# Kernel optimization log

Hardware: AMD Instinct MI355X
Metric: run time of the kernel (lower is better)

Reference implementation:

```python
import jax, jax.numpy as jnp
import numpy as np

B, P, K, L, F, KS, NCLS = 8, 4096, 20, 10, 32, 5, 40
N = B * P


def setup_inputs() -> dict:
    key = jax.random.key(0)
    k = jax.random.split(key, 5)
    return {
        "pos": jax.random.normal(k[0], (N, 3), jnp.float32),
        "Wsp": jax.random.normal(k[1], (KS ** 3, F), jnp.float32) * 0.1,
        "root": jax.random.normal(k[2], (F,), jnp.float32) * 0.1,
        "bias": jnp.zeros((F,), jnp.float32),
        "gamma": jnp.ones((F,), jnp.float32),
        "beta": jnp.zeros((F,), jnp.float32),
        "W1": jax.random.normal(k[3], (F, 256), jnp.float32) * 0.1,
        "b1": jnp.zeros((256,), jnp.float32),
        "W2": jax.random.normal(k[4], (256, NCLS), jnp.float32) * 0.1,
        "b2": jnp.zeros((NCLS,), jnp.float32),
    }


def _knn(pos):
    # per-graph brute-force knn (loop=False), neighbors sorted by distance
    pts = pos.reshape(B, P, 3)

    def one(p):
        d = jnp.sum((p[:, None, :] - p[None, :, :]) ** 2, -1)  # (P,P)
        d = d.at[jnp.arange(P), jnp.arange(P)].set(jnp.inf)
        return jax.lax.top_k(-d, K)[1]

    nbr = jax.vmap(one)(pts) + (jnp.arange(B) * P)[:, None, None]
    return nbr.reshape(N, K)


def _eig3(A):
    # power iteration with deflation (nr_iterations=5) on batched 3x3 symmetric mats
    def pi(M):
        v = jnp.full((M.shape[0], 3), np.float32(3.0 ** -0.5))
        for _ in range(5):
            v = jnp.einsum("nij,nj->ni", M, v)
            v = v / (jnp.linalg.norm(v, axis=-1, keepdims=True) + 1e-12)
        lam = jnp.einsum("ni,nij,nj->n", v, M, v)
        return lam, v

    l1, v1 = pi(A)
    _, v2 = pi(A - l1[:, None, None] * v1[:, :, None] * v1[:, None, :])
    v3 = jnp.cross(v1, v2)
    v3 = v3 / (jnp.linalg.norm(v3, axis=-1, keepdims=True) + 1e-12)
    return jnp.stack([v1, v2, v3], axis=1)  # rows = eigenvectors, V[:,2] = normal


def reference(pos, Wsp, root, bias, gamma, beta, W1, b1, W2, b2):
    nbr = _knn(pos)                               # (N,K)
    clusters = pos[nbr] - pos[:, None, :]         # (N,K,3) neighbor - center
    cov = jnp.einsum("nmc,nmd->ncd", clusters[:, :L], clusters[:, :L])
    V = _eig3(cov)                                # (N,3,3)
    dirc = jnp.einsum("nkc,ndc->nkd", clusters, V)  # clusters @ V^T
    signs = jnp.sign(dirc[:, :, 2].sum(1))
    dirc = dirc.at[:, :, 2].multiply(signs[:, None])
    max_abs = jnp.max(jnp.abs(dirc).reshape(N, -1), 1)
    dirc = dirc / max_abs[:, None, None] * 0.5 + 0.5  # pseudo coords in [0,1]

    # SplineConv, degree=1, open splines, dim=3, in_channels=1 (x=ones)
    v = dirc * (KS - 1)
    f = jnp.floor(v)
    frac = v - f
    fi = f.astype(jnp.int32)
    bits = jnp.array([[(s >> 2) & 1, (s >> 1) & 1, s & 1] for s in range(8)], jnp.int32)
    idx = jnp.clip(fi[:, :, None, :] + bits[None, None, :, :], 0, KS - 1)  # (N,K,8,3)
    wgt = jnp.where(bits[None, None] == 1, frac[:, :, None, :], 1.0 - frac[:, :, None, :])
    basis = wgt.prod(-1)                                          # (N,K,8)
    flat = (idx[..., 0] * KS + idx[..., 1]) * KS + idx[..., 2]    # (N,K,8)
    msg = jnp.einsum("nks,nksf->nf", basis, Wsp[flat]) / K        # mean aggregation
    node = msg + root + bias                                      # root weight on x=1

    # BatchNorm1d (training-mode batch stats, eps=1e-5)
    mu = node.mean(0)
    var = ((node - mu) ** 2).mean(0)
    xb = gamma * (node - mu) / jnp.sqrt(var + 1e-5) + beta

    out3 = xb[:, :, None] * V[:, 2][:, None, :]   # (N,F,3) scale normal direction
    y = jax.nn.sigmoid(out3)
    ys = y.reshape(-1, P, F).mean(1)              # (3B,F) as in torch .view
    y1 = jax.nn.elu(ys @ W1 + b1)
    return jax.nn.log_softmax(y1 @ W2 + b2, axis=1)
```

## Files before the change

### kernel.cpp

```cpp
#include <hip/hip_runtime.h>
#include <hip/hip_bf16.h>
#include <math.h>

#define BGR 8
#define PP 4096
#define NPTS 32768
#define KNN 20
#define LCOV 10
#define FF 32
#define KS 5
#define NCLS 40
#define NGROUP 24
#define GROUPLEN 131072

#define SPLIT 8
#define CHUNK (PP / SPLIT)
#define PTSBLK 128
#define KTHR 1024
#define NSLOT (KNN + 1)
#define MPAD NSLOT
#define SENT 0xFFFFFFFFu
#define SCELLS 4096
#define SCAP 12

__device__ inline unsigned umn(unsigned a, unsigned b) { return a < b ? a : b; }
__device__ inline unsigned umx(unsigned a, unsigned b) { return a > b ? a : b; }

__device__ inline void mat3vec(const float M[9], const float v[3], float w[3]) {
    w[0] = M[0] * v[0] + M[1] * v[1] + M[2] * v[2];
    w[1] = M[3] * v[0] + M[4] * v[1] + M[5] * v[2];
    w[2] = M[6] * v[0] + M[7] * v[1] + M[8] * v[2];
}

__device__ inline float pi3(const float M[9], float v[3]) {
    v[0] = v[1] = v[2] = 0.57735026918962576f;
#pragma unroll
    for (int it = 0; it < 5; ++it) {
        float w[3];
        mat3vec(M, v, w);
        float nrm = sqrtf(w[0] * w[0] + w[1] * w[1] + w[2] * w[2]) + 1e-12f;
        v[0] = w[0] / nrm;
        v[1] = w[1] / nrm;
        v[2] = w[2] / nrm;
    }
    float w[3];
    mat3vec(M, v, w);
    return v[0] * w[0] + v[1] * w[1] + v[2] * w[2];
}

__global__ __launch_bounds__(KTHR, 4) void knn_kernel(
    const float* __restrict__ pos, unsigned short* __restrict__ nbr16,
    float* __restrict__ Rbuf, float* __restrict__ v3out) {
    __shared__ float smem[4 * PP];
    __shared__ unsigned short mOrig[PP];
    __shared__ unsigned samp[PTSBLK * 24];
    __shared__ float Tseed[PTSBLK];
    __shared__ unsigned scr[KTHR / 64][SCAP][64];
    float* tx = smem;
    float* ty = smem + PP;
    float* tz = smem + 2 * PP;
    float* tw = smem + 3 * PP;
    unsigned short* lnbr = (unsigned short*)(smem + 3 * PP + 2816);

    int b = blockIdx.x >> 5;
    int blkInGraph = blockIdx.x & 31;
    const float* gp = pos + (size_t)b * PP * 3;
    int tid = threadIdx.x;
    int lane = tid & 63;
    int wid = tid >> 6;

    {
        unsigned* cnt = (unsigned*)smem;
        unsigned short* cellOf = (unsigned short*)(smem + 4096);
        unsigned* tsum = (unsigned*)(smem + 6144);
        for (int i = tid; i < SCELLS; i += KTHR) cnt[i] = 0u;
        __syncthreads();
        for (int i = tid; i < PP; i += KTHR) {
            float x = gp[i * 3 + 0];
            float y = gp[i * 3 + 1];
            float z = gp[i * 3 + 2];
            int cx = min(max((int)floorf((x + 4.0f) * 2.0f), 0), 15);
            int cy = min(max((int)floorf((y + 4.0f) * 2.0f), 0), 15);
            int cz = min(max((int)floorf((z + 4.0f) * 2.0f), 0), 15);
            unsigned m = 0;
#pragma unroll
            for (int bb = 0; bb < 4; ++bb)
                m |= (((unsigned)(cx >> bb) & 1u) << (3 * bb + 2)) |
                     (((unsigned)(cy >> bb) & 1u) << (3 * bb + 1)) |
                     (((unsigned)(cz >> bb) & 1u) << (3 * bb + 0));
            cellOf[i] = (unsigned short)m;
            atomicAdd(&cnt[m], 1u);
        }
        __syncthreads();
        unsigned c0 = cnt[4 * tid + 0];
        unsigned c1 = cnt[4 * tid + 1];
        unsigned c2 = cnt[4 * tid + 2];
        unsigned c3 = cnt[4 * tid + 3];
        unsigned local = c0 + c1 + c2 + c3;
        tsum[tid] = local;
        __syncthreads();
        for (int off = 1; off < 1024; off <<= 1) {
            unsigned v = (tid >= off) ? tsum[tid - off] : 0u;
            __syncthreads();
            tsum[tid] += v;
            __syncthreads();
        }
        unsigned base = tsum[tid] - local;
        cnt[4 * tid + 0] = base;
        cnt[4 * tid + 1] = base + c0;
        cnt[4 * tid + 2] = base + c0 + c1;
        cnt[4 * tid + 3] = base + c0 + c1 + c2;
        __syncthreads();
        for (int i = tid; i < PP; i += KTHR) {
            unsigned dst = atomicAdd(&cnt[cellOf[i]], 1u);
            mOrig[dst] = (unsigned short)i;
        }
    }
    __syncthreads();

    for (int i = tid; i < PP; i += KTHR) {
        float x = gp[i * 3 + 0];
        float y = gp[i * 3 + 1];
        float z = gp[i * 3 + 2];
        tx[i] = -2.0f * x;
        ty[i] = -2.0f * y;
        tz[i] = -2.0f * z;
        tw[i] = x * x + y * y + z * z;
    }
    __syncthreads();

    int eighth = tid >> 7;
    int pt = tid & (PTSBLK - 1);
    int qSlot = blkInGraph * PTSBLK + pt;
    int li = mOrig[qSlot];
    float px = -0.5f * tx[li];
    float py = -0.5f * ty[li];
    float pz = -0.5f * tz[li];
    float p2 = tw[li];
    int jbeg = eighth * CHUNK;

    {
        unsigned s0 = SENT, s1 = SENT, s2 = SENT;
#pragma unroll 4
        for (int c = 0; c < 32; ++c) {
            int base = jbeg + c * 16;
            float4 xv = *(const float4*)(tx + base);
            float4 yv = *(const float4*)(ty + base);
            float4 zv = *(const float4*)(tz + base);
            float4 wv = *(const float4*)(tw + base);
            float xa[4] = {xv.x, xv.y, xv.z, xv.w};
            float ya[4] = {yv.x, yv.y, yv.z, yv.w};
            float za[4] = {zv.x, zv.y, zv.z, zv.w};
            float wa[4] = {wv.x, wv.y, wv.z, wv.w};
#pragma unroll
            for (int u = 0; u < 4; ++u) {
                float dh = fmaf(px, xa[u], fmaf(py, ya[u], fmaf(pz, za[u], wa[u])));
                float d = fmaxf(dh + p2, 0.0f);
                unsigned key = (__float_as_uint(d) & 0xFFFFF000u)
                               | (unsigned)(base + u);
                if (base + u == li) key = SENT;
                unsigned t0 = umn(key, s0); key = umx(key, s0); s0 = t0;
                t0 = umn(key, s1); key = umx(key, s1); s1 = t0;
                s2 = umn(key, s2);
            }
        }
        unsigned* sdst = &samp[pt * 24 + eighth * 3];
        sdst[0] = s0; sdst[1] = s1; sdst[2] = s2;
    }
    __syncthreads();
    if (tid < PTSBLK) {
        unsigned g0 = 0, g1 = 0, g2 = 0, g3 = 0;
        const unsigned* ss = &samp[tid * 24];
#pragma unroll
        for (int i = 0; i < 24; ++i) {
            unsigned k = ss[i], a;
            a = umx(k, g0); k = umn(k, g0); g0 = a;
            a = umx(k, g1); k = umn(k, g1); g1 = a;
            a = umx(k, g2); k = umn(k, g2); g2 = a;
            g3 = umx(k, g3);
        }
        Tseed[tid] = __uint_as_float((g3 & 0xFFFFF000u) + 0x2000u);
    }
    __syncthreads();
    float seed_hat = Tseed[pt] - p2;

    unsigned bd[NSLOT];
#pragma unroll
    for (int k = 0; k < NSLOT; k++) bd[k] = SENT;
    float worst_hat = seed_hat;

    unsigned* scrW = &scr[wid][0][0];
    unsigned cnt = 0;

    auto drain = [&]() {
#pragma unroll
        for (int s = 0; s < SCAP; ++s) {
            if (!__any((int)cnt > s)) break;
            unsigned k = (s < (int)cnt) ? scrW[s * 64 + lane] : SENT;
#pragma unroll
            for (int i = 0; i < NSLOT; i++) {
                unsigned lo = umn(k, bd[i]);
                k = umx(k, bd[i]);
                bd[i] = lo;
            }
        }
        cnt = 0;
        unsigned wb = bd[NSLOT - 1];
        float nw = (wb == SENT) ? INFINITY
                                : __uint_as_float(wb & 0xFFFFF000u) - p2;
        worst_hat = fminf(nw, seed_hat);
    };

    for (int jj = jbeg; jj < jbeg + CHUNK; jj += 8) {
        float4 xv0 = *(const float4*)(tx + jj);
        float4 yv0 = *(const float4*)(ty + jj);
        float4 zv0 = *(const float4*)(tz + jj);
        float4 wv0 = *(const float4*)(tw + jj);
        float4 xv1 = *(const float4*)(tx + jj + 4);
        float4 yv1 = *(const float4*)(ty + jj + 4);
        float4 zv1 = *(const float4*)(tz + jj + 4);
        float4 wv1 = *(const float4*)(tw + jj + 4);
        float xa[8] = {xv0.x, xv0.y, xv0.z, xv0.w, xv1.x, xv1.y, xv1.z, xv1.w};
        float ya[8] = {yv0.x, yv0.y, yv0.z, yv0.w, yv1.x, yv1.y, yv1.z, yv1.w};
        float za[8] = {zv0.x, zv0.y, zv0.z, zv0.w, zv1.x, zv1.y, zv1.z, zv1.w};
        float wa[8] = {wv0.x, wv0.y, wv0.z, wv0.w, wv1.x, wv1.y, wv1.z, wv1.w};
#pragma unroll
        for (int u = 0; u < 8; u++) {
            float dh = fmaf(px, xa[u], fmaf(py, ya[u], fmaf(pz, za[u], wa[u])));
            if (dh < worst_hat) {
                float d = fmaxf(dh + p2, 0.0f);
                scrW[cnt * 64 + lane] = (__float_as_uint(d) & 0xFFFFF000u)
                                        | (unsigned)(jj + u);
                cnt++;
            }
        }
        if (__any(cnt >= 4u)) drain();
    }
    drain();

    __syncthreads();
    unsigned* mk = (unsigned*)smem;
    for (int h = 0; h < 2; h++) {
        if ((pt >> 6) == h) {
            int lpt = pt & 63;
#pragma unroll
            for (int k = 0; k < NSLOT; k++)
                mk[(eighth * 64 + lpt) * MPAD + k] = bd[k];
        }
        __syncthreads();
        if (tid < 64) {
            int p = tid;
            const unsigned* base = &mk[p * MPAD];
            int cur[SPLIT];
#pragma unroll
            for (int q = 0; q < SPLIT; q++) cur[q] = 0;
            int lpt2 = h * 64 + p;
            int gi = b * PP + (int)mOrig[blkInGraph * PTSBLK + lpt2];
#pragma unroll
            for (int t = 0; t < NSLOT; t++) {
                unsigned v[SPLIT];
#pragma unroll
                for (int q = 0; q < SPLIT; q++)
                    v[q] = base[q * 64 * MPAD + cur[q]];
                unsigned m = v[0];
#pragma unroll
                for (int q = 1; q < SPLIT; q++) m = umn(m, v[q]);
                if (t > 0) {
                    int local = (int)(m & 0xFFFu);
                    nbr16[(size_t)gi * KNN + (t - 1)] = (unsigned short)local;
                    lnbr[lpt2 * KNN + (t - 1)] = (unsigned short)local;
                }
#pragma unroll
                for (int q = 0; q < SPLIT; q++) cur[q] += (v[q] == m);
            }
        }
        __syncthreads();
    }

    for (int i = tid; i < PP; i += KTHR) {
        tx[i] = gp[i * 3 + 0];
        ty[i] = gp[i * 3 + 1];
        tz[i] = gp[i * 3 + 2];
    }
    __syncthreads();

    if (tid < PTSBLK) {
        int lp = tid;
        int ng = mOrig[blkInGraph * PTSBLK + lp];
        int n = b * PP + ng;
        float qx = tx[ng], qy = ty[ng], qz = tz[ng];
        const unsigned short* ln = &lnbr[lp * KNN];

        float m00 = 0.f, m01 = 0.f, m02 = 0.f, m11 = 0.f, m12 = 0.f, m22 = 0.f;
#pragma unroll
        for (int k = 0; k < LCOV; k++) {
            int id = ln[k];
            float cx = tx[id] - qx;
            float cy = ty[id] - qy;
            float cz = tz[id] - qz;
            m00 += cx * cx; m01 += cx * cy; m02 += cx * cz;
            m11 += cy * cy; m12 += cy * cz; m22 += cz * cz;
        }
        float M[9] = {m00, m01, m02, m01, m11, m12, m02, m12, m22};

        float v1[3], v2[3], v3[3];
        float l1 = pi3(M, v1);
        float M2[9];
#pragma unroll
        for (int c = 0; c < 3; c++)
#pragma unroll
            for (int d = 0; d < 3; d++)
                M2[c * 3 + d] = M[c * 3 + d] - l1 * v1[c] * v1[d];
        pi3(M2, v2);
        v3[0] = v1[1] * v2[2] - v1[2] * v2[1];
        v3[1] = v1[2] * v2[0] - v1[0] * v2[2];
        v3[2] = v1[0] * v2[1] - v1[1] * v2[0];
        {
            float nrm = sqrtf(v3[0] * v3[0] + v3[1] * v3[1] + v3[2] * v3[2]) + 1e-12f;
            v3[0] /= nrm; v3[1] /= nrm; v3[2] /= nrm;
        }

        float ssum = 0.f, mx = 0.f;
#pragma unroll
        for (int k = 0; k < KNN; k++) {
            int id = ln[k];
            float cx = tx[id] - qx;
            float cy = ty[id] - qy;
            float cz = tz[id] - qz;
            float d0 = cx * v1[0] + cy * v1[1] + cz * v1[2];
            float d1 = cx * v2[0] + cy * v2[1] + cz * v2[2];
            float d2 = cx * v3[0] + cy * v3[1] + cz * v3[2];
            ssum += d2;
            mx = fmaxf(mx, fabsf(d0));
            mx = fmaxf(mx, fabsf(d1));
            mx = fmaxf(mx, fabsf(d2));
        }
        float sgn = (ssum > 0.f) ? 1.f : ((ssum < 0.f) ? -1.f : 0.f);

        float sc = 2.0f / mx;
        float* R = Rbuf + (size_t)n * 12;
        R[0] = v1[0] * sc;  R[1] = v1[1] * sc;  R[2] = v1[2] * sc;
        R[3] = v2[0] * sc;  R[4] = v2[1] * sc;  R[5] = v2[2] * sc;
        float s2 = sgn * sc;
        R[6] = v3[0] * s2;  R[7] = v3[1] * s2;  R[8] = v3[2] * s2;
        R[9] = 0.f; R[10] = 0.f; R[11] = 0.f;

        v3out[n * 3 + 0] = v3[0];
        v3out[n * 3 + 1] = v3[1];
        v3out[n * 3 + 2] = v3[2];
    }
}

#define NPB 16
#define SPLBLKS (NPTS / NPB)
__global__ __launch_bounds__(512) void spline_kernel(
    const float* __restrict__ pos, const unsigned short* __restrict__ nbr16,
    const float* __restrict__ Rbuf, const float* __restrict__ Wsp,
    const float* __restrict__ root, const float* __restrict__ bias,
    float* __restrict__ node, float* __restrict__ sums_part) {
    __shared__ float wbuf[NPB * KNN * 8];

    int tid = threadIdx.x;
    if (tid < NPB * KNN) {
        int pt = tid / KNN;
        int k = tid - pt * KNN;
        int n = blockIdx.x * NPB + pt;
        const float4* Rv = (const float4*)(Rbuf + (size_t)n * 12);
        float4 r0 = Rv[0], r1 = Rv[1], r2 = Rv[2];
        float px = pos[n * 3 + 0], py = pos[n * 3 + 1], pz = pos[n * 3 + 2];
        int id = (n & ~(PP - 1)) | (int)nbr16[(size_t)n * KNN + k];
        float cxx = pos[id * 3 + 0] - px;
        float cyy = pos[id * 3 + 1] - py;
        float czz = pos[id * 3 + 2] - pz;
        float v0 = fmaf(cxx, r0.x, fmaf(cyy, r0.y, fmaf(czz, r0.z, 2.0f)));
        float v1 = fmaf(cxx, r0.w, fmaf(cyy, r1.x, fmaf(czz, r1.y, 2.0f)));
        float v2 = fmaf(cxx, r1.z, fmaf(cyy, r1.w, fmaf(czz, r2.x, 2.0f)));
        float f0 = floorf(v0), f1 = floorf(v1), f2 = floorf(v2);
        float fr0 = v0 - f0, fr1 = v1 - f1, fr2 = v2 - f2;
        int fi0 = (int)f0, fi1 = (int)f1, fi2 = (int)f2;
        float* wdst = &wbuf[(pt * KNN + k) * 8];
#pragma unroll
        for (int s = 0; s < 8; s++) {
            int b0 = (s >> 2) & 1, b1 = (s >> 1) & 1, b2s = s & 1;
            int i0 = min(max(fi0 + b0, 0), KS - 1);
            int i1 = min(max(fi1 + b1, 0), KS - 1);
            int i2 = min(max(fi2 + b2s, 0), KS - 1);
            float w = (b0 ? fr0 : 1.f - fr0) * (b1 ? fr1 : 1.f - fr1) *
                      (b2s ? fr2 : 1.f - fr2);
            unsigned flat = (unsigned)((i0 * KS + i1) * KS + i2);
            wdst[s] = __uint_as_float((__float_as_uint(w) & ~127u) | flat);
        }
    }
    __syncthreads();

    int pt = tid >> 5;
    int f = tid & 31;
    const float* wrow = &wbuf[pt * (KNN * 8)];
    float acc = 0.f;
#pragma unroll
    for (int k = 0; k < KNN; k++) {
        float4 wa = *(const float4*)&wrow[k * 8];
        float4 wb = *(const float4*)&wrow[k * 8 + 4];
        float wv[8] = {wa.x, wa.y, wa.z, wa.w, wb.x, wb.y, wb.z, wb.w};
#pragma unroll
        for (int s = 0; s < 8; s++) {
            unsigned u = __float_as_uint(wv[s]) & 127u;
            acc = fmaf(wv[s], Wsp[u * FF + f], acc);
        }
    }
    int n = blockIdx.x * NPB + pt;
    float val = acc * (1.0f / KNN) + root[f] + bias[f];
    node[(size_t)n * FF + f] = val;

    __syncthreads();
    wbuf[tid] = val;
    wbuf[512 + tid] = val * val;
    __syncthreads();
    if (tid < 64) {
        int ff = tid & 31;
        int off = (tid >> 5) * 512;
        float s = 0.f;
#pragma unroll
        for (int p = 0; p < NPB; p++) s += wbuf[off + p * 32 + ff];
        sums_part[(size_t)blockIdx.x * 64 + tid] = s;
    }
}

#define YSPLIT 8
#define YCHUNK (GROUPLEN / YSPLIT)
__global__ __launch_bounds__(256) void ys_kernel(
    const float* __restrict__ node, const float* __restrict__ v3,
    const float* __restrict__ sums_part, const float* __restrict__ gamma,
    const float* __restrict__ beta, float* __restrict__ ys_part) {
    __shared__ float stat4[256];
    __shared__ float stat[64];
    __shared__ float sa[FF], sb[FF];
    {
        int col = threadIdx.x & 63;
        int q = threadIdx.x >> 6;
        float s0 = 0.f, s1 = 0.f, s2 = 0.f, s3 = 0.f;
        for (int p = q * 512; p < (q + 1) * 512; p += 4) {
            s0 += sums_part[(p + 0) * 64 + col];
            s1 += sums_part[(p + 1) * 64 + col];
            s2 += sums_part[(p + 2) * 64 + col];
            s3 += sums_part[(p + 3) * 64 + col];
        }
        stat4[threadIdx.x] = (s0 + s1) + (s2 + s3);
    }
    __syncthreads();
    if (threadIdx.x < 64) {
        stat[threadIdx.x] = stat4[threadIdx.x] + stat4[64 + threadIdx.x] +
                            stat4[128 + threadIdx.x] + stat4[192 + threadIdx.x];
    }
    __syncthreads();
    if (threadIdx.x < FF) {
        int f = threadIdx.x;
        float mu = stat[f] * (1.0f / NPTS);
        float var = stat[FF + f] * (1.0f / NPTS) - mu * mu;
        float inv = 1.0f / sqrtf(var + 1e-5f);
        sa[f] = gamma[f] * inv;
        sb[f] = beta[f] - gamma[f] * inv * mu;
    }
    __syncthreads();

    int g = blockIdx.x >> 3;
    int sub = blockIdx.x & 7;
    int t0 = g * GROUPLEN + sub * YCHUNK + threadIdx.x;
    int n = t0 / 96;
    int r0 = t0 - n * 96;
    int rj[3], fj[3], cj[3], dj[3];
    rj[0] = r0;
    rj[1] = (r0 + 64) % 96;
    rj[2] = (r0 + 32) % 96;
#pragma unroll
    for (int j = 0; j < 3; j++) {
        fj[j] = rj[j] / 3;
        cj[j] = rj[j] - fj[j] * 3;
        dj[j] = (rj[j] >= 32) ? 3 : 2;
    }
    float Sa0 = sa[fj[0]], Sb0 = sb[fj[0]];
    float Sa1 = sa[fj[1]], Sb1 = sb[fj[1]];
    float Sa2 = sa[fj[2]], Sb2 = sb[fj[2]];
    int nf = n * FF;
    int n3 = n * 3;

    float acc = 0.f;
#pragma unroll 1
    for (int tr = 0; tr < 21; tr++) {
        {
            float xb = fmaf(Sa0, node[nf + fj[0]], Sb0);
            float val = xb * v3[n3 + cj[0]];
            acc += 1.0f / (1.0f + __expf(-val));
            nf += dj[0] * FF; n3 += dj[0] * 3;
        }
        {
            float xb = fmaf(Sa1, node[nf + fj[1]], Sb1);
            float val = xb * v3[n3 + cj[1]];
            acc += 1.0f / (1.0f + __expf(-val));
            nf += dj[1] * FF; n3 += dj[1] * 3;
        }
        {
            float xb = fmaf(Sa2, node[nf + fj[2]], Sb2);
            float val = xb * v3[n3 + cj[2]];
            acc += 1.0f / (1.0f + __expf(-val));
            nf += dj[2] * FF; n3 += dj[2] * 3;
        }
    }
    {
        float xb = fmaf(Sa0, node[nf + fj[0]], Sb0);
        float val = xb * v3[n3 + cj[0]];
        acc += 1.0f / (1.0f + __expf(-val));
    }

    __shared__ float red[256];
    red[threadIdx.x] = acc;
    __syncthreads();
    if (threadIdx.x < FF) {
        float s = 0.f;
        for (int t = threadIdx.x; t < 256; t += FF) s += red[t];
        ys_part[(sub * NGROUP + g) * FF + threadIdx.x] = s * (1.0f / PP);
    }
}

__global__ __launch_bounds__(256) void head_kernel(
    const float* __restrict__ ys_part, const float* __restrict__ W1,
    const float* __restrict__ b1, const float* __restrict__ W2,
    const float* __restrict__ b2, float* __restrict__ out) {
    int g = blockIdx.x;
    __shared__ float syr[FF];
    __shared__ float h[256];
    __shared__ float logits[NCLS];
    __shared__ float mstat[2];
    if (threadIdx.x < FF) {
        float s = 0.f;
#pragma unroll
        for (int sub = 0; sub < YSPLIT; sub++)
            s += ys_part[(sub * NGROUP + g) * FF + threadIdx.x];
        syr[threadIdx.x] = s;
    }
    __syncthreads();
    int j = threadIdx.x;
    float acc = b1[j];
#pragma unroll
    for (int f = 0; f < FF; f++) acc += syr[f] * W1[f * 256 + j];
    h[j] = acc > 0.f ? acc : expm1f(acc);
    __syncthreads();
    if (j < NCLS) {
        float l = b2[j];
        for (int q = 0; q < 256; q++) l += h[q] * W2[q * NCLS + j];
        logits[j] = l;
    }
    __syncthreads();
    if (j == 0) {
        float m = -INFINITY;
        for (int o = 0; o < NCLS; o++) m = fmaxf(m, logits[o]);
        float s = 0.f;
        for (int o = 0; o < NCLS; o++) s += expf(logits[o] - m);
        mstat[0] = m;
        mstat[1] = logf(s);
    }
    __syncthreads();
    if (j < NCLS) out[g * NCLS + j] = logits[j] - mstat[0] - mstat[1];
}

extern "C" void kernel_launch(void* const* d_in, const int* in_sizes, int n_in,
                              void* d_out, int out_size, void* d_ws, size_t ws_size,
                              hipStream_t stream) {
    const float* pos   = (const float*)d_in[0];
    const float* Wsp   = (const float*)d_in[1];
    const float* root  = (const float*)d_in[2];
    const float* bias  = (const float*)d_in[3];
    const float* gamma = (const float*)d_in[4];
    const float* beta  = (const float*)d_in[5];
    const float* W1    = (const float*)d_in[6];
    const float* b1    = (const float*)d_in[7];
    const float* W2    = (const float*)d_in[8];
    const float* b2    = (const float*)d_in[9];
    float* out = (float*)d_out;

    char* ws = (char*)d_ws;
    unsigned short* nbr16 = (unsigned short*)(ws);
    float* sums_part = (float*)(ws + 1310720);
    float* ys_part   = (float*)(ws + 1835008);
    float* node = (float*)(ws + 2621440);
    float* v3   = (float*)(ws + 6815744);
    float* Rbuf = (float*)(ws + 7212288);

    knn_kernel<<<256, KTHR, 0, stream>>>(pos, nbr16, Rbuf, v3);
    spline_kernel<<<SPLBLKS, 512, 0, stream>>>(pos, nbr16, Rbuf, Wsp, root,
                                               bias, node, sums_part);
    ys_kernel<<<NGROUP * YSPLIT, 256, 0, stream>>>(node, v3, sums_part, gamma,
                                                   beta, ys_part);
    head_kernel<<<NGROUP, 256, 0, stream>>>(ys_part, W1, b1, W2, b2, out);
}
```

Measured before the change: 200.3 us.

## Accumulate BatchNorm stats via atomics and split ys kernel into more blocks

The spline kernel now atomically adds its per-block feature sums and sums of squares into a single 64-float accumulator, zeroed by a memset, instead of writing 2048 partial rows. This removes the redundant reduction that every ys_kernel block previously did over the whole partial-sum array. In addition, ys_kernel is split 32 ways per group instead of 8 (loop trip count reduced accordingly) to expose more parallelism. The trade-offs are heavy atomic contention on 64 addresses, non-deterministic float summation order, and one extra memset launch.

```diff
diff --git a/kernel.cpp b/kernel.cpp
--- a/kernel.cpp
+++ b/kernel.cpp
@@ -357,7 +357,7 @@
     const float* __restrict__ pos, const unsigned short* __restrict__ nbr16,
     const float* __restrict__ Rbuf, const float* __restrict__ Wsp,
     const float* __restrict__ root, const float* __restrict__ bias,
-    float* __restrict__ node, float* __restrict__ sums_part) {
+    float* __restrict__ node, float* __restrict__ sums_accum) {
     __shared__ float wbuf[NPB * KNN * 8];
 
     int tid = threadIdx.x;
@@ -422,49 +422,29 @@
         float s = 0.f;
 #pragma unroll
         for (int p = 0; p < NPB; p++) s += wbuf[off + p * 32 + ff];
-        sums_part[(size_t)blockIdx.x * 64 + tid] = s;
-    }
-}
-
-#define YSPLIT 8
+        atomicAdd(&sums_accum[tid], s);
+    }
+}
+
+#define YSPLIT 32
 #define YCHUNK (GROUPLEN / YSPLIT)
 __global__ __launch_bounds__(256) void ys_kernel(
     const float* __restrict__ node, const float* __restrict__ v3,
-    const float* __restrict__ sums_part, const float* __restrict__ gamma,
+    const float* __restrict__ sums_accum, const float* __restrict__ gamma,
     const float* __restrict__ beta, float* __restrict__ ys_part) {
-    __shared__ float stat4[256];
-    __shared__ float stat[64];
     __shared__ float sa[FF], sb[FF];
-    {
-        int col = threadIdx.x & 63;
-        int q = threadIdx.x >> 6;
-        float s0 = 0.f, s1 = 0.f, s2 = 0.f, s3 = 0.f;
-        for (int p = q * 512; p < (q + 1) * 512; p += 4) {
-            s0 += sums_part[(p + 0) * 64 + col];
-            s1 += sums_part[(p + 1) * 64 + col];
-            s2 += sums_part[(p + 2) * 64 + col];
-            s3 += sums_part[(p + 3) * 64 + col];
-        }
-        stat4[threadIdx.x] = (s0 + s1) + (s2 + s3);
-    }
-    __syncthreads();
-    if (threadIdx.x < 64) {
-        stat[threadIdx.x] = stat4[threadIdx.x] + stat4[64 + threadIdx.x] +
-                            stat4[128 + threadIdx.x] + stat4[192 + threadIdx.x];
-    }
-    __syncthreads();
     if (threadIdx.x < FF) {
         int f = threadIdx.x;
-        float mu = stat[f] * (1.0f / NPTS);
-        float var = stat[FF + f] * (1.0f / NPTS) - mu * mu;
+        float mu = sums_accum[f] * (1.0f / NPTS);
+        float var = sums_accum[FF + f] * (1.0f / NPTS) - mu * mu;
         float inv = 1.0f / sqrtf(var + 1e-5f);
         sa[f] = gamma[f] * inv;
         sb[f] = beta[f] - gamma[f] * inv * mu;
     }
     __syncthreads();
 
-    int g = blockIdx.x >> 3;
-    int sub = blockIdx.x & 7;
+    int g = blockIdx.x >> 5;
+    int sub = blockIdx.x & 31;
     int t0 = g * GROUPLEN + sub * YCHUNK + threadIdx.x;
     int n = t0 / 96;
     int r0 = t0 - n * 96;
@@ -486,7 +466,7 @@
 
     float acc = 0.f;
 #pragma unroll 1
-    for (int tr = 0; tr < 21; tr++) {
+    for (int tr = 0; tr < 5; tr++) {
         {
             float xb = fmaf(Sa0, node[nf + fj[0]], Sb0);
             float val = xb * v3[n3 + cj[0]];
@@ -580,16 +560,17 @@
 
     char* ws = (char*)d_ws;
     unsigned short* nbr16 = (unsigned short*)(ws);
-    float* sums_part = (float*)(ws + 1310720);
+    float* sums_accum = (float*)(ws + 1310720);
     float* ys_part   = (float*)(ws + 1835008);
     float* node = (float*)(ws + 2621440);
     float* v3   = (float*)(ws + 6815744);
     float* Rbuf = (float*)(ws + 7212288);
 
+    hipMemsetAsync(sums_accum, 0, 64 * sizeof(float), stream);
     knn_kernel<<<256, KTHR, 0, stream>>>(pos, nbr16, Rbuf, v3);
     spline_kernel<<<SPLBLKS, 512, 0, stream>>>(pos, nbr16, Rbuf, Wsp, root,
-                                               bias, node, sums_part);
-    ys_kernel<<<NGROUP * YSPLIT, 256, 0, stream>>>(node, v3, sums_part, gamma,
+                                               bias, node, sums_accum);
+    ys_kernel<<<NGROUP * YSPLIT, 256, 0, stream>>>(node, v3, sums_accum, gamma,
                                                    beta, ys_part);
     head_kernel<<<NGROUP, 256, 0, stream>>>(ys_part, W1, b1, W2, b2, out);
 }
```

Result: slower. 219.1 us (+9.4%).
